# Optimization experiments

Measured on AMD Instinct MI355X. Metric: run time of the kernel, lower is better.

Reference implementation:

```python
import jax, jax.numpy as jnp
import numpy as np

BLOCK = 64
EPS = 1e-6
N_HEADS = 16


def _rope(t, cos, sin):
    # t: (B,S,H,hd); cos/sin: (S, hd//2) -> broadcast (1,S,1,hd//2)
    B, S, H, hd = t.shape
    tr = t.reshape(B, S, H, hd // 2, 2)
    t0, t1 = tr[..., 0], tr[..., 1]
    c = cos[None, :, None, :]
    s = sin[None, :, None, :]
    o0 = t0 * c - t1 * s
    o1 = t0 * s + t1 * c
    return jnp.stack([o0, o1], axis=-1).reshape(B, S, H, hd)


def setup_inputs() -> dict:
    key = jax.random.key(0)
    ks = jax.random.split(key, 6)
    B, S, D = 1, 2048, 2048
    hd = D // N_HEADS
    x = jax.random.normal(ks[0], (B, S, D), dtype=jnp.float32)
    # rotary table: theta_i = 10000^(-2i/hd)
    inv_freq = 1.0 / (10000.0 ** (jnp.arange(0, hd, 2, dtype=jnp.float32) / hd))
    t = jnp.arange(S, dtype=jnp.float32)
    freqs = jnp.outer(t, inv_freq)  # (S, hd//2)
    freqs_cos = jnp.cos(freqs)
    freqs_sin = jnp.sin(freqs)
    std = 0.02
    Wq = jax.random.normal(ks[1], (D, D), dtype=jnp.float32) * std
    Wk = jax.random.normal(ks[2], (D, D), dtype=jnp.float32) * std
    Wv = jax.random.normal(ks[3], (D, D), dtype=jnp.float32) * std
    Wo = jax.random.normal(ks[4], (D, D), dtype=jnp.float32) * std
    mask = jnp.ones((1, 1), dtype=bool)  # non-None mask => no masking in original code
    return {"x": x, "freqs_cos": freqs_cos, "freqs_sin": freqs_sin,
            "Wq": Wq, "Wk": Wk, "Wv": Wv, "Wo": Wo, "mask": mask}


def reference(x, freqs_cos, freqs_sin, Wq, Wk, Wv, Wo, mask):
    B, S, D = x.shape
    H = N_HEADS
    hd = D // H
    scale = hd ** -0.5
    nb = S // BLOCK

    q = (x @ Wq.T).reshape(B, S, H, hd)
    k = (x @ Wk.T).reshape(B, S, H, hd)
    v = (x @ Wv.T).reshape(B, S, H, hd)
    q = _rope(q, freqs_cos, freqs_sin)
    k = _rope(k, freqs_cos, freqs_sin)

    # block views: (B, nb, BLOCK, H, hd)
    qb = q.reshape(B, nb, BLOCK, H, hd)
    kb = k.reshape(B, nb, BLOCK, H, hd)
    vb = v.reshape(B, nb, BLOCK, H, hd)

    # per-(i,j) block scores: (B, nb_i, nb_j, H, BLOCK_q, BLOCK_k)
    s = jnp.einsum('binhd,bjmhd->bijhnm', qb, kb) * scale
    # NOTE: original module (mask is not None path) applies NO causal mask and
    # uses the per-block local max (no running-max rescale) -- reproduced exactly.
    m = jnp.max(s, axis=-1, keepdims=True)
    p = jnp.exp(s - m)
    # denominator: sum of per-block row sums over all j blocks -> (B, nb, H, BLOCK)
    L = p.sum(axis=-1).sum(axis=2)
    # numerator: sum over j blocks of p @ v -> (B, nb, BLOCK, H, hd)
    O = jnp.einsum('bijhnm,bjmhd->binhd', p, vb).reshape(B, S, H, hd)
    Lr = L.transpose(0, 1, 3, 2).reshape(B, S, H, 1)  # (B,S,H,1)
    O = O / (Lr + EPS)
    return O.reshape(B, S, D) @ Wo.T
```

## Files before the change

kernel.cpp:

```cpp
#include <hip/hip_runtime.h>
#include <hip/hip_bf16.h>
#include <math.h>

#define SEQ 2048
#define DM  2048
#define NH  16
#define HD  128
#define SCALE 0.08838834764831845f

typedef __bf16 bf16_t;
typedef __bf16 bf16x8 __attribute__((ext_vector_type(8)));
typedef __bf16 bf16x4 __attribute__((ext_vector_type(4)));
typedef float  f32x4  __attribute__((ext_vector_type(4)));

typedef const __attribute__((address_space(1))) void* gas_ptr;
typedef __attribute__((address_space(3))) void* las_ptr;

__device__ __forceinline__ void gload_lds16(const void* g, void* l) {
    __builtin_amdgcn_global_load_lds((gas_ptr)g, (las_ptr)l, 16, 0, 0);
}

__device__ __forceinline__ f32x4 mfma_bf16(bf16x8 a, bf16x8 b, f32x4 c) {
    return __builtin_amdgcn_mfma_f32_16x16x32_bf16(a, b, c, 0, 0, 0);
}

__device__ __forceinline__ bf16x8 read_frag64(const bf16_t* lds, int row, int k) {
    int chunk = (k >> 3) ^ (row & 7);
    return *(const bf16x8*)(lds + row * 64 + chunk * 8);
}
__device__ __forceinline__ bf16x8 read_frag128(const bf16_t* lds, int row, int k) {
    int chunk = k >> 3;
    chunk = (chunk & 8) | ((chunk ^ row) & 7);
    return *(const bf16x8*)(lds + row * 128 + chunk * 8);
}
__device__ __forceinline__ bf16x8 read_frag32(const bf16_t* lds, int row, int k) {
    int L = row >> 1;
    int u = ((row & 1) << 2) | (k >> 3);
    int c = u ^ (L & 7);
    return *(const bf16x8*)(lds + ((L << 3) + c) * 8);
}

__global__ __launch_bounds__(256) void cvt5(
    const float* __restrict__ s0, const float* __restrict__ s1,
    const float* __restrict__ s2, const float* __restrict__ s3,
    const float* __restrict__ s4,
    bf16_t* __restrict__ d0, bf16_t* __restrict__ d1, bf16_t* __restrict__ d2,
    bf16_t* __restrict__ d3, bf16_t* __restrict__ d4)
{
    int which = blockIdx.y;
    const float* s; bf16_t* d;
    switch (which) {
        case 0: s = s0; d = d0; break;
        case 1: s = s1; d = d1; break;
        case 2: s = s2; d = d2; break;
        case 3: s = s3; d = d3; break;
        default: s = s4; d = d4; break;
    }
    size_t idx = ((size_t)blockIdx.x * 256 + threadIdx.x) * 4;
    float4 v = *(const float4*)(s + idx);
    bf16x4 o = { (bf16_t)v.x, (bf16_t)v.y, (bf16_t)v.z, (bf16_t)v.w };
    *(bf16x4*)(d + idx) = o;
}

__global__ __launch_bounds__(512, 2) void qkv_pipe(
    const bf16_t* __restrict__ A,
    const bf16_t* __restrict__ B0, const bf16_t* __restrict__ B1,
    const bf16_t* __restrict__ B2,
    bf16_t* __restrict__ Oq, bf16_t* __restrict__ Ok, bf16_t* __restrict__ Ov,
    const float* __restrict__ fcos, const float* __restrict__ fsin)
{
    __shared__ bf16_t lds3[49152];

    const int tid = threadIdx.x;
    const int lane = tid & 63;
    const int w = tid >> 6;
    const int wm = w >> 2;
    const int wn = w & 3;
    const int g = lane >> 4, r15 = lane & 15;

    const int bm = blockIdx.x;
    const int bny = blockIdx.y;
    const int sel = bny >> 3;
    const int bnl = bny & 7;
    const bf16_t* Bp = (sel == 0) ? B0 : (sel == 1) ? B1 : B2;

    const size_t arow0 = (size_t)bm * 256;
    const size_t brow0 = (size_t)bnl * 256;

    int ci0 = tid, ci1 = 512 + tid;
    int L0 = ci0 >> 3, u0 = (ci0 & 7) ^ (L0 & 7);
    int L1 = ci1 >> 3, u1 = (ci1 & 7) ^ (L1 & 7);
    int mrow0 = (L0 << 1) | (u0 >> 2), kc0 = u0 & 3;
    int mrow1 = (L1 << 1) | (u1 >> 2), kc1 = u1 & 3;
    const bf16_t* gA0 = A  + (arow0 + mrow0) * DM + kc0 * 8;
    const bf16_t* gA1 = A  + (arow0 + mrow1) * DM + kc1 * 8;
    const bf16_t* gB0 = Bp + (brow0 + mrow0) * DM + kc0 * 8;
    const bf16_t* gB1 = Bp + (brow0 + mrow1) * DM + kc1 * 8;
    const int dst0 = (0 * 512 + w * 64) * 16;
    const int dst1 = (1 * 512 + w * 64) * 16;

    const int NT = DM / 32;

    f32x4 acc[8][4] = {};

    {
        char* s0a = (char*)(lds3);
        char* s0b = (char*)(lds3 + 8192);
        char* s1a = (char*)(lds3 + 16384);
        char* s1b = (char*)(lds3 + 16384 + 8192);
        gload_lds16(gA0 + 0 * 32, s0a + dst0);
        gload_lds16(gB0 + 0 * 32, s0b + dst0);
        gload_lds16(gA1 + 0 * 32, s0a + dst1);
        gload_lds16(gB1 + 0 * 32, s0b + dst1);
        gload_lds16(gA0 + 1 * 32, s1a + dst0);
        gload_lds16(gB0 + 1 * 32, s1b + dst0);
        gload_lds16(gA1 + 1 * 32, s1a + dst1);
        gload_lds16(gB1 + 1 * 32, s1b + dst1);
    }
    asm volatile("s_waitcnt vmcnt(4)" ::: "memory");
    __builtin_amdgcn_s_barrier();

    int sk = 0, sp = 2;
    for (int k = 0; k < NT; ++k) {
        const bf16_t* sA = lds3 + sk * 16384;
        const bf16_t* sB = sA + 8192;
        char* pA = (char*)(lds3 + sp * 16384);
        char* pB = pA + 8192 * 2;
        const bool pf = (k + 2 < NT);
        const int kO = (k + 2) * 32;

        bf16x8 afrag[4], bfrag[4];
        #pragma unroll
        for (int m = 0; m < 4; ++m)
            afrag[m] = read_frag32(sA, wm * 128 + m * 16 + r15, g * 8);
        #pragma unroll
        for (int n = 0; n < 4; ++n)
            bfrag[n] = read_frag32(sB, wn * 64 + n * 16 + r15, g * 8);
        if (pf) {
            gload_lds16(gA0 + kO, pA + dst0);
            gload_lds16(gB0 + kO, pB + dst0);
        }
        __builtin_amdgcn_s_barrier();
        __builtin_amdgcn_s_setprio(1);
        #pragma unroll
        for (int m = 0; m < 4; ++m)
            #pragma unroll
            for (int n = 0; n < 4; ++n)
                acc[m][n] = mfma_bf16(afrag[m], bfrag[n], acc[m][n]);
        __builtin_amdgcn_s_setprio(0);
        __builtin_amdgcn_s_barrier();

        #pragma unroll
        for (int m = 0; m < 4; ++m)
            afrag[m] = read_frag32(sA, wm * 128 + (m + 4) * 16 + r15, g * 8);
        if (pf) {
            gload_lds16(gA1 + kO, pA + dst1);
            gload_lds16(gB1 + kO, pB + dst1);
        }
        if (k < NT - 2) asm volatile("s_waitcnt vmcnt(4)" ::: "memory");
        else            asm volatile("s_waitcnt vmcnt(0)" ::: "memory");
        __builtin_amdgcn_s_barrier();
        __builtin_amdgcn_s_setprio(1);
        #pragma unroll
        for (int m = 0; m < 4; ++m)
            #pragma unroll
            for (int n = 0; n < 4; ++n)
                acc[m + 4][n] = mfma_bf16(afrag[m], bfrag[n], acc[m + 4][n]);
        __builtin_amdgcn_s_setprio(0);
        __builtin_amdgcn_s_barrier();

        sk = (sk == 2) ? 0 : sk + 1;
        sp = (sp == 2) ? 0 : sp + 1;
    }

    const int r0 = bm * 256 + wm * 128;
    const int c0 = bnl * 256 + wn * 64;

    if (sel == 2) {
        #pragma unroll
        for (int m = 0; m < 8; ++m) {
            int rowb = r0 + m * 16 + g * 4;
            #pragma unroll
            for (int n = 0; n < 4; ++n) {
                int col = c0 + n * 16 + r15;
                bf16x4 pk = { (bf16_t)acc[m][n][0], (bf16_t)acc[m][n][1],
                              (bf16_t)acc[m][n][2], (bf16_t)acc[m][n][3] };
                *(bf16x4*)&Ov[(size_t)col * SEQ + rowb] = pk;
            }
        }
    } else {
        bf16_t* dst = (sel == 0) ? Oq : Ok;
        #pragma unroll
        for (int m = 0; m < 8; ++m) {
            int rowb = r0 + m * 16 + g * 4;
            #pragma unroll
            for (int n = 0; n < 4; ++n) {
                int col = c0 + n * 16 + r15;
                int f = (col & (HD - 1)) >> 1;
                float sgn = (col & 1) ? 1.0f : -1.0f;
                #pragma unroll
                for (int r = 0; r < 4; ++r) {
                    float mine = acc[m][n][r];
                    float other = __shfl_xor(mine, 1);
                    float cc = fcos[(rowb + r) * (HD / 2) + f];
                    float ss = fsin[(rowb + r) * (HD / 2) + f];
                    float o = mine * cc + sgn * other * ss;
                    dst[(size_t)(rowb + r) * DM + col] = (bf16_t)o;
                }
            }
        }
    }
}

template<int MODE>
__global__ __launch_bounds__(256) void gemm_k(
    const bf16_t* __restrict__ A,
    const bf16_t* __restrict__ B0, const bf16_t* __restrict__ B1,
    const bf16_t* __restrict__ B2,
    bf16_t* __restrict__ Oq, bf16_t* __restrict__ Ok, bf16_t* __restrict__ Ov,
    float* __restrict__ Of,
    const float* __restrict__ fcos, const float* __restrict__ fsin)
{
    __shared__ bf16_t lA[128 * 64];
    __shared__ bf16_t lB[128 * 64];

    const int tid = threadIdx.x;
    const int lane = tid & 63;
    const int w = tid >> 6;
    const int wm = w >> 1, wn = w & 1;
    const int g = lane >> 4, r15 = lane & 15;

    const int bm = blockIdx.x;
    int sel, bn;
    const bf16_t* Bp;
    if (MODE == 0) {
        int bny = blockIdx.y;
        sel = bny >> 4; bn = bny & 15;
        Bp = (sel == 0) ? B0 : (sel == 1) ? B1 : B2;
    } else {
        sel = 3; bn = blockIdx.y; Bp = B0;
    }

    f32x4 acc[4][4] = {};

    const size_t arow0 = (size_t)bm * 128;
    const size_t brow0 = (size_t)bn * 128;

    for (int kt = 0; kt < DM / 64; ++kt) {
        const int k0 = kt * 64;
        #pragma unroll
        for (int i = 0; i < 4; ++i) {
            int c = i * 256 + tid;
            int row = c >> 3;
            int ck = (c ^ row) & 7;
            const bf16_t* ga = A + (arow0 + row) * DM + k0 + ck * 8;
            gload_lds16(ga, (char*)lA + (i * 256 + w * 64) * 16);
            const bf16_t* gb = Bp + (brow0 + row) * DM + k0 + ck * 8;
            gload_lds16(gb, (char*)lB + (i * 256 + w * 64) * 16);
        }
        __syncthreads();
        #pragma unroll
        for (int kk = 0; kk < 2; ++kk) {
            bf16x8 af[4], bfr[4];
            #pragma unroll
            for (int m = 0; m < 4; ++m)
                af[m] = read_frag64(lA, wm * 64 + m * 16 + r15, kk * 32 + g * 8);
            #pragma unroll
            for (int n = 0; n < 4; ++n)
                bfr[n] = read_frag64(lB, wn * 64 + n * 16 + r15, kk * 32 + g * 8);
            #pragma unroll
            for (int m = 0; m < 4; ++m)
                #pragma unroll
                for (int n = 0; n < 4; ++n)
                    acc[m][n] = mfma_bf16(af[m], bfr[n], acc[m][n]);
        }
        __syncthreads();
    }

    const int r0 = bm * 128 + wm * 64;
    const int c0 = bn * 128 + wn * 64;

    if (MODE == 1) {
        #pragma unroll
        for (int m = 0; m < 4; ++m) {
            int rowb = r0 + m * 16 + g * 4;
            #pragma unroll
            for (int n = 0; n < 4; ++n) {
                int col = c0 + n * 16 + r15;
                #pragma unroll
                for (int r = 0; r < 4; ++r)
                    Of[(size_t)(rowb + r) * DM + col] = acc[m][n][r];
            }
        }
    }
}

__global__ __launch_bounds__(256) void attn_k(
    const bf16_t* __restrict__ Q, const bf16_t* __restrict__ Kb,
    const bf16_t* __restrict__ Vt, bf16_t* __restrict__ Ob)
{
    __shared__ bf16_t lq[64 * 128];
    __shared__ bf16_t lk[64 * 128];
    __shared__ bf16_t lv[128 * 64];
    __shared__ bf16_t lp[64 * 64];

    const int tid = threadIdx.x;
    const int lane = tid & 63;
    const int w = tid >> 6;
    const int g = lane >> 4, r15 = lane & 15;
    const int qb = blockIdx.x, h = blockIdx.y;

    #pragma unroll
    for (int i = 0; i < 4; ++i) {
        int c = i * 256 + tid;
        int row = c >> 4, ckl = c & 15;
        int ck = (ckl & 8) | ((ckl ^ row) & 7);
        const bf16_t* gq = Q + (size_t)(qb * 64 + row) * DM + h * HD + ck * 8;
        gload_lds16(gq, (char*)lq + (i * 256 + w * 64) * 16);
    }

    f32x4 oacc[8] = {};
    float Lp[4] = {0.f, 0.f, 0.f, 0.f};
    __syncthreads();

    for (int j = 0; j < SEQ / 64; ++j) {
        #pragma unroll
        for (int i = 0; i < 4; ++i) {
            int c = i * 256 + tid;
            int row = c >> 4, ckl = c & 15;
            int ck = (ckl & 8) | ((ckl ^ row) & 7);
            const bf16_t* gk = Kb + (size_t)(j * 64 + row) * DM + h * HD + ck * 8;
            gload_lds16(gk, (char*)lk + (i * 256 + w * 64) * 16);
        }
        #pragma unroll
        for (int i = 0; i < 4; ++i) {
            int c = i * 256 + tid;
            int row = c >> 3;
            int ck = (c ^ row) & 7;
            const bf16_t* gv = Vt + (size_t)(h * HD + row) * SEQ + j * 64 + ck * 8;
            gload_lds16(gv, (char*)lv + (i * 256 + w * 64) * 16);
        }
        __syncthreads();

        f32x4 sacc[4] = {};
        #pragma unroll
        for (int ks = 0; ks < 4; ++ks) {
            bf16x8 aq = read_frag128(lq, w * 16 + r15, ks * 32 + g * 8);
            #pragma unroll
            for (int n = 0; n < 4; ++n) {
                bf16x8 bk = read_frag128(lk, n * 16 + r15, ks * 32 + g * 8);
                sacc[n] = mfma_bf16(aq, bk, sacc[n]);
            }
        }

        float p[4][4];
        #pragma unroll
        for (int r = 0; r < 4; ++r) {
            float mx = fmaxf(fmaxf(sacc[0][r], sacc[1][r]),
                             fmaxf(sacc[2][r], sacc[3][r]));
            mx = fmaxf(mx, __shfl_xor(mx, 1));
            mx = fmaxf(mx, __shfl_xor(mx, 2));
            mx = fmaxf(mx, __shfl_xor(mx, 4));
            mx = fmaxf(mx, __shfl_xor(mx, 8));
            #pragma unroll
            for (int n = 0; n < 4; ++n) {
                float pv = __expf((sacc[n][r] - mx) * SCALE);
                p[n][r] = pv;
                Lp[r] += pv;
            }
        }
        #pragma unroll
        for (int n = 0; n < 4; ++n)
            #pragma unroll
            for (int r = 0; r < 4; ++r) {
                int row = w * 16 + g * 4 + r;
                int col = n * 16 + r15;
                int chunk = (col >> 3) ^ (row & 7);
                lp[row * 64 + chunk * 8 + (col & 7)] = (bf16_t)p[n][r];
            }

        #pragma unroll
        for (int ks = 0; ks < 2; ++ks) {
            bf16x8 ap = read_frag64(lp, w * 16 + r15, ks * 32 + g * 8);
            #pragma unroll
            for (int n = 0; n < 8; ++n) {
                bf16x8 bv = read_frag64(lv, n * 16 + r15, ks * 32 + g * 8);
                oacc[n] = mfma_bf16(ap, bv, oacc[n]);
            }
        }
        __syncthreads();
    }

    #pragma unroll
    for (int r = 0; r < 4; ++r) {
        float L = Lp[r];
        L += __shfl_xor(L, 1);
        L += __shfl_xor(L, 2);
        L += __shfl_xor(L, 4);
        L += __shfl_xor(L, 8);
        Lp[r] = 1.0f / (L + 1e-6f);
    }
    #pragma unroll
    for (int n = 0; n < 8; ++n) {
        int col = h * HD + n * 16 + r15;
        int rowb = qb * 64 + w * 16 + g * 4;
        #pragma unroll
        for (int r = 0; r < 4; ++r)
            Ob[(size_t)(rowb + r) * DM + col] = (bf16_t)(oacc[n][r] * Lp[r]);
    }
}

extern "C" void kernel_launch(void* const* d_in, const int* in_sizes, int n_in,
                              void* d_out, int out_size, void* d_ws, size_t ws_size,
                              hipStream_t stream)
{
    const float* x    = (const float*)d_in[0];
    const float* fcos = (const float*)d_in[1];
    const float* fsin = (const float*)d_in[2];
    const float* Wq   = (const float*)d_in[3];
    const float* Wk   = (const float*)d_in[4];
    const float* Wv   = (const float*)d_in[5];
    const float* Wo   = (const float*)d_in[6];
    float* out = (float*)d_out;

    const size_t NE = (size_t)DM * SEQ;
    bf16_t* ws  = (bf16_t*)d_ws;
    bf16_t* xb  = ws;
    bf16_t* wqb = ws + 1 * NE;
    bf16_t* wkb = ws + 2 * NE;
    bf16_t* wvb = ws + 3 * NE;
    bf16_t* wob = ws + 4 * NE;
    bf16_t* qr  = ws + 5 * NE;
    bf16_t* kr  = ws + 6 * NE;
    bf16_t* vt  = ws + 7 * NE;
    bf16_t* ob  = ws + 8 * NE;

    hipLaunchKernelGGL(cvt5, dim3(4096, 5), dim3(256), 0, stream,
                       x, Wq, Wk, Wv, Wo, xb, wqb, wkb, wvb, wob);

    hipLaunchKernelGGL(qkv_pipe, dim3(8, 24), dim3(512), 0, stream,
                       xb, wqb, wkb, wvb, qr, kr, vt, fcos, fsin);

    hipLaunchKernelGGL(attn_k, dim3(32, 16), dim3(256), 0, stream,
                       qr, kr, vt, ob);

    hipLaunchKernelGGL(HIP_KERNEL_NAME(gemm_k<1>), dim3(16, 16), dim3(256), 0, stream,
                       ob, wob, (bf16_t*)nullptr, (bf16_t*)nullptr,
                       (bf16_t*)nullptr, (bf16_t*)nullptr, (bf16_t*)nullptr,
                       out, fcos, fsin);
}
```

Baseline: 203.6 us.

## Restructure attention kernel with register Q, transposed S, double-buffered KV, shuffled P

The attention kernel now runs 8 waves over 128 query rows per block and keeps Q fragments in registers instead of LDS. It computes S transposed (K as the A operand) so that row reductions become cross-lane shuffles. P is packed to bf16 and redistributed by lane shuffles rather than a round trip through LDS. K/V tiles are double-buffered, prefetching the next block while computing the current one, with setprio raised around the MFMA sections. The gemm template is also simplified into a dedicated final-projection kernel. This removes LDS traffic and per-iteration load stalls at the cost of more registers and fewer, larger blocks.

```diff
diff --git a/kernel.cpp b/kernel.cpp
--- a/kernel.cpp
+++ b/kernel.cpp
@@ -12,6 +12,7 @@
 typedef __bf16 bf16x8 __attribute__((ext_vector_type(8)));
 typedef __bf16 bf16x4 __attribute__((ext_vector_type(4)));
 typedef float  f32x4  __attribute__((ext_vector_type(4)));
+typedef int    i32x4  __attribute__((ext_vector_type(4)));
 
 typedef const __attribute__((address_space(1))) void* gas_ptr;
 typedef __attribute__((address_space(3))) void* las_ptr;
@@ -22,6 +23,12 @@
 
 __device__ __forceinline__ f32x4 mfma_bf16(bf16x8 a, bf16x8 b, f32x4 c) {
     return __builtin_amdgcn_mfma_f32_16x16x32_bf16(a, b, c, 0, 0, 0);
+}
+
+__device__ __forceinline__ unsigned cvtpk_bf16(float lo, float hi) {
+    unsigned d;
+    asm("v_cvt_pk_bf16_f32 %0, %1, %2" : "=v"(d) : "v"(lo), "v"(hi));
+    return d;
 }
 
 __device__ __forceinline__ bf16x8 read_frag64(const bf16_t* lds, int row, int k) {
@@ -212,14 +219,9 @@
     }
 }
 
-template<int MODE>
-__global__ __launch_bounds__(256) void gemm_k(
-    const bf16_t* __restrict__ A,
-    const bf16_t* __restrict__ B0, const bf16_t* __restrict__ B1,
-    const bf16_t* __restrict__ B2,
-    bf16_t* __restrict__ Oq, bf16_t* __restrict__ Ok, bf16_t* __restrict__ Ov,
-    float* __restrict__ Of,
-    const float* __restrict__ fcos, const float* __restrict__ fsin)
+__global__ __launch_bounds__(256) void gemm_fin(
+    const bf16_t* __restrict__ A, const bf16_t* __restrict__ B0,
+    float* __restrict__ Of)
 {
     __shared__ bf16_t lA[128 * 64];
     __shared__ bf16_t lB[128 * 64];
@@ -231,15 +233,7 @@
     const int g = lane >> 4, r15 = lane & 15;
 
     const int bm = blockIdx.x;
-    int sel, bn;
-    const bf16_t* Bp;
-    if (MODE == 0) {
-        int bny = blockIdx.y;
-        sel = bny >> 4; bn = bny & 15;
-        Bp = (sel == 0) ? B0 : (sel == 1) ? B1 : B2;
-    } else {
-        sel = 3; bn = blockIdx.y; Bp = B0;
-    }
+    const int bn = blockIdx.y;
 
     f32x4 acc[4][4] = {};
 
@@ -255,7 +249,7 @@
             int ck = (c ^ row) & 7;
             const bf16_t* ga = A + (arow0 + row) * DM + k0 + ck * 8;
             gload_lds16(ga, (char*)lA + (i * 256 + w * 64) * 16);
-            const bf16_t* gb = Bp + (brow0 + row) * DM + k0 + ck * 8;
+            const bf16_t* gb = B0 + (brow0 + row) * DM + k0 + ck * 8;
             gload_lds16(gb, (char*)lB + (i * 256 + w * 64) * 16);
         }
         __syncthreads();
@@ -279,30 +273,25 @@
 
     const int r0 = bm * 128 + wm * 64;
     const int c0 = bn * 128 + wn * 64;
-
-    if (MODE == 1) {
-        #pragma unroll
-        for (int m = 0; m < 4; ++m) {
-            int rowb = r0 + m * 16 + g * 4;
-            #pragma unroll
-            for (int n = 0; n < 4; ++n) {
-                int col = c0 + n * 16 + r15;
-                #pragma unroll
-                for (int r = 0; r < 4; ++r)
-                    Of[(size_t)(rowb + r) * DM + col] = acc[m][n][r];
-            }
-        }
-    }
-}
-
-__global__ __launch_bounds__(256) void attn_k(
+    #pragma unroll
+    for (int m = 0; m < 4; ++m) {
+        int rowb = r0 + m * 16 + g * 4;
+        #pragma unroll
+        for (int n = 0; n < 4; ++n) {
+            int col = c0 + n * 16 + r15;
+            #pragma unroll
+            for (int r = 0; r < 4; ++r)
+                Of[(size_t)(rowb + r) * DM + col] = acc[m][n][r];
+        }
+    }
+}
+
+__global__ __launch_bounds__(512, 2) void attn_k2(
     const bf16_t* __restrict__ Q, const bf16_t* __restrict__ Kb,
     const bf16_t* __restrict__ Vt, bf16_t* __restrict__ Ob)
 {
-    __shared__ bf16_t lq[64 * 128];
-    __shared__ bf16_t lk[64 * 128];
-    __shared__ bf16_t lv[128 * 64];
-    __shared__ bf16_t lp[64 * 64];
+    __shared__ bf16_t lk[2 * 64 * 128];
+    __shared__ bf16_t lv[2 * 128 * 64];
 
     const int tid = threadIdx.x;
     const int lane = tid & 63;
@@ -310,103 +299,139 @@
     const int g = lane >> 4, r15 = lane & 15;
     const int qb = blockIdx.x, h = blockIdx.y;
 
-    #pragma unroll
-    for (int i = 0; i < 4; ++i) {
-        int c = i * 256 + tid;
-        int row = c >> 4, ckl = c & 15;
-        int ck = (ckl & 8) | ((ckl ^ row) & 7);
-        const bf16_t* gq = Q + (size_t)(qb * 64 + row) * DM + h * HD + ck * 8;
-        gload_lds16(gq, (char*)lq + (i * 256 + w * 64) * 16);
+    const int lo = g & 1, hb = g >> 1;
+    const int e_src = (lo << 5) + r15;
+    const int o_src = e_src + 16;
+    const int sA = hb ? o_src : e_src;
+    const int sB = hb ? e_src : o_src;
+
+    bf16x8 qf[4];
+    {
+        const bf16_t* qrow = Q + (size_t)(qb * 128 + w * 16 + r15) * DM + h * HD + g * 8;
+        #pragma unroll
+        for (int ks = 0; ks < 4; ++ks)
+            qf[ks] = *(const bf16x8*)(qrow + ks * 32);
     }
 
     f32x4 oacc[8] = {};
-    float Lp[4] = {0.f, 0.f, 0.f, 0.f};
-    __syncthreads();
+    float Lsum = 0.f;
+
+    #define STAGE_KV(JJ, BUF)                                                     \
+    {                                                                             \
+        _Pragma("unroll")                                                         \
+        for (int i = 0; i < 2; ++i) {                                             \
+            int c = i * 512 + tid;                                                \
+            int row = c >> 4, ckl = c & 15;                                       \
+            int ck = (ckl & 8) | ((ckl ^ row) & 7);                               \
+            const bf16_t* gk = Kb + (size_t)((JJ) * 64 + row) * DM + h * HD + ck * 8; \
+            gload_lds16(gk, (char*)lk + (BUF) * 16384 + (i * 512 + w * 64) * 16); \
+        }                                                                         \
+        _Pragma("unroll")                                                         \
+        for (int i = 0; i < 2; ++i) {                                             \
+            int c = i * 512 + tid;                                                \
+            int row = c >> 3;                                                     \
+            int ck = (c ^ row) & 7;                                               \
+            const bf16_t* gv = Vt + (size_t)(h * HD + row) * SEQ + (JJ) * 64 + ck * 8; \
+            gload_lds16(gv, (char*)lv + (BUF) * 16384 + (i * 512 + w * 64) * 16); \
+        }                                                                         \
+    }
+
+    STAGE_KV(0, 0);
+    asm volatile("s_waitcnt vmcnt(0)" ::: "memory");
+    __builtin_amdgcn_s_barrier();
 
     for (int j = 0; j < SEQ / 64; ++j) {
-        #pragma unroll
-        for (int i = 0; i < 4; ++i) {
-            int c = i * 256 + tid;
-            int row = c >> 4, ckl = c & 15;
-            int ck = (ckl & 8) | ((ckl ^ row) & 7);
-            const bf16_t* gk = Kb + (size_t)(j * 64 + row) * DM + h * HD + ck * 8;
-            gload_lds16(gk, (char*)lk + (i * 256 + w * 64) * 16);
-        }
-        #pragma unroll
-        for (int i = 0; i < 4; ++i) {
-            int c = i * 256 + tid;
-            int row = c >> 3;
-            int ck = (c ^ row) & 7;
-            const bf16_t* gv = Vt + (size_t)(h * HD + row) * SEQ + j * 64 + ck * 8;
-            gload_lds16(gv, (char*)lv + (i * 256 + w * 64) * 16);
-        }
-        __syncthreads();
+        const int cur = j & 1;
+        const bf16_t* lkc = lk + cur * 8192;
+        const bf16_t* lvc = lv + cur * 8192;
+        if (j < SEQ / 64 - 1) STAGE_KV(j + 1, cur ^ 1);
 
         f32x4 sacc[4] = {};
+        __builtin_amdgcn_s_setprio(1);
         #pragma unroll
         for (int ks = 0; ks < 4; ++ks) {
-            bf16x8 aq = read_frag128(lq, w * 16 + r15, ks * 32 + g * 8);
             #pragma unroll
             for (int n = 0; n < 4; ++n) {
-                bf16x8 bk = read_frag128(lk, n * 16 + r15, ks * 32 + g * 8);
-                sacc[n] = mfma_bf16(aq, bk, sacc[n]);
+                bf16x8 kf = read_frag128(lkc, n * 16 + r15, ks * 32 + g * 8);
+                sacc[n] = mfma_bf16(kf, qf[ks], sacc[n]);
             }
         }
+        __builtin_amdgcn_s_setprio(0);
+
+        float mx0 = fmaxf(fmaxf(sacc[0][0], sacc[0][1]), fmaxf(sacc[0][2], sacc[0][3]));
+        float mx1 = fmaxf(fmaxf(sacc[1][0], sacc[1][1]), fmaxf(sacc[1][2], sacc[1][3]));
+        float mx2 = fmaxf(fmaxf(sacc[2][0], sacc[2][1]), fmaxf(sacc[2][2], sacc[2][3]));
+        float mx3 = fmaxf(fmaxf(sacc[3][0], sacc[3][1]), fmaxf(sacc[3][2], sacc[3][3]));
+        float mx = fmaxf(fmaxf(mx0, mx1), fmaxf(mx2, mx3));
+        mx = fmaxf(mx, __shfl_xor(mx, 16));
+        mx = fmaxf(mx, __shfl_xor(mx, 32));
 
         float p[4][4];
-        #pragma unroll
-        for (int r = 0; r < 4; ++r) {
-            float mx = fmaxf(fmaxf(sacc[0][r], sacc[1][r]),
-                             fmaxf(sacc[2][r], sacc[3][r]));
-            mx = fmaxf(mx, __shfl_xor(mx, 1));
-            mx = fmaxf(mx, __shfl_xor(mx, 2));
-            mx = fmaxf(mx, __shfl_xor(mx, 4));
-            mx = fmaxf(mx, __shfl_xor(mx, 8));
-            #pragma unroll
-            for (int n = 0; n < 4; ++n) {
+        float ls = 0.f;
+        #pragma unroll
+        for (int n = 0; n < 4; ++n)
+            #pragma unroll
+            for (int r = 0; r < 4; ++r) {
                 float pv = __expf((sacc[n][r] - mx) * SCALE);
                 p[n][r] = pv;
-                Lp[r] += pv;
+                ls += pv;
             }
-        }
-        #pragma unroll
-        for (int n = 0; n < 4; ++n)
-            #pragma unroll
-            for (int r = 0; r < 4; ++r) {
-                int row = w * 16 + g * 4 + r;
-                int col = n * 16 + r15;
-                int chunk = (col >> 3) ^ (row & 7);
-                lp[row * 64 + chunk * 8 + (col & 7)] = (bf16_t)p[n][r];
-            }
-
-        #pragma unroll
-        for (int ks = 0; ks < 2; ++ks) {
-            bf16x8 ap = read_frag64(lp, w * 16 + r15, ks * 32 + g * 8);
-            #pragma unroll
-            for (int n = 0; n < 8; ++n) {
-                bf16x8 bv = read_frag64(lv, n * 16 + r15, ks * 32 + g * 8);
-                oacc[n] = mfma_bf16(ap, bv, oacc[n]);
-            }
-        }
-        __syncthreads();
-    }
-
+        Lsum += ls;
+
+        unsigned D00 = cvtpk_bf16(p[0][0], p[0][1]), D01 = cvtpk_bf16(p[0][2], p[0][3]);
+        unsigned D10 = cvtpk_bf16(p[1][0], p[1][1]), D11 = cvtpk_bf16(p[1][2], p[1][3]);
+        unsigned D20 = cvtpk_bf16(p[2][0], p[2][1]), D21 = cvtpk_bf16(p[2][2], p[2][3]);
+        unsigned D30 = cvtpk_bf16(p[3][0], p[3][1]), D31 = cvtpk_bf16(p[3][2], p[3][3]);
+
+        unsigned r0 = __shfl((int)(lo ? D10 : D00), sA);
+        unsigned r1 = __shfl((int)(lo ? D11 : D01), sA);
+        unsigned r2 = __shfl((int)(lo ? D00 : D10), sB);
+        unsigned r3 = __shfl((int)(lo ? D01 : D11), sB);
+        unsigned r4 = __shfl((int)(lo ? D30 : D20), sA);
+        unsigned r5 = __shfl((int)(lo ? D31 : D21), sA);
+        unsigned r6 = __shfl((int)(lo ? D20 : D30), sB);
+        unsigned r7 = __shfl((int)(lo ? D21 : D31), sB);
+        i32x4 w0, w1;
+        w0[0] = (int)(hb ? r2 : r0);  w0[1] = (int)(hb ? r3 : r1);
+        w0[2] = (int)(hb ? r0 : r2);  w0[3] = (int)(hb ? r1 : r3);
+        w1[0] = (int)(hb ? r6 : r4);  w1[1] = (int)(hb ? r7 : r5);
+        w1[2] = (int)(hb ? r4 : r6);  w1[3] = (int)(hb ? r5 : r7);
+        bf16x8 pa0 = __builtin_bit_cast(bf16x8, w0);
+        bf16x8 pa1 = __builtin_bit_cast(bf16x8, w1);
+
+        __builtin_amdgcn_s_setprio(1);
+        #pragma unroll
+        for (int n = 0; n < 8; ++n) {
+            bf16x8 bv = read_frag64(lvc, n * 16 + r15, g * 8);
+            oacc[n] = mfma_bf16(pa0, bv, oacc[n]);
+        }
+        #pragma unroll
+        for (int n = 0; n < 8; ++n) {
+            bf16x8 bv = read_frag64(lvc, n * 16 + r15, 32 + g * 8);
+            oacc[n] = mfma_bf16(pa1, bv, oacc[n]);
+        }
+        __builtin_amdgcn_s_setprio(0);
+
+        asm volatile("s_waitcnt vmcnt(0)" ::: "memory");
+        __builtin_amdgcn_s_barrier();
+    }
+
+    float L = Lsum;
+    L += __shfl_xor(L, 16);
+    L += __shfl_xor(L, 32);
+    float inv = 1.0f / (L + 1e-6f);
+    float invr[4];
     #pragma unroll
-    for (int r = 0; r < 4; ++r) {
-        float L = Lp[r];
-        L += __shfl_xor(L, 1);
-        L += __shfl_xor(L, 2);
-        L += __shfl_xor(L, 4);
-        L += __shfl_xor(L, 8);
-        Lp[r] = 1.0f / (L + 1e-6f);
-    }
+    for (int r = 0; r < 4; ++r)
+        invr[r] = __shfl(inv, g * 4 + r);
+
     #pragma unroll
     for (int n = 0; n < 8; ++n) {
         int col = h * HD + n * 16 + r15;
-        int rowb = qb * 64 + w * 16 + g * 4;
+        int rowb = qb * 128 + w * 16 + g * 4;
         #pragma unroll
         for (int r = 0; r < 4; ++r)
-            Ob[(size_t)(rowb + r) * DM + col] = (bf16_t)(oacc[n][r] * Lp[r]);
+            Ob[(size_t)(rowb + r) * DM + col] = (bf16_t)(oacc[n][r] * invr[r]);
     }
 }
 
@@ -441,11 +466,9 @@
     hipLaunchKernelGGL(qkv_pipe, dim3(8, 24), dim3(512), 0, stream,
                        xb, wqb, wkb, wvb, qr, kr, vt, fcos, fsin);
 
-    hipLaunchKernelGGL(attn_k, dim3(32, 16), dim3(256), 0, stream,
+    hipLaunchKernelGGL(attn_k2, dim3(16, 16), dim3(512), 0, stream,
                        qr, kr, vt, ob);
 
-    hipLaunchKernelGGL(HIP_KERNEL_NAME(gemm_k<1>), dim3(16, 16), dim3(256), 0, stream,
-                       ob, wob, (bf16_t*)nullptr, (bf16_t*)nullptr,
-                       (bf16_t*)nullptr, (bf16_t*)nullptr, (bf16_t*)nullptr,
-                       out, fcos, fsin);
-}
+    hipLaunchKernelGGL(gemm_fin, dim3(16, 16), dim3(256), 0, stream,
+                       ob, wob, out);
+}
```

Result: faster. 189.1 us (-7.1%).
